# Optimization experiments

Hardware: AMD Instinct MI355X
Metric: run time of the kernel (lower is better)

Reference implementation:

```python
import jax, jax.numpy as jnp
import numpy as np

MAX_K_QK = 64
MAX_K_V = 64
MAX_K_KNOW = 128


def threshold_gate(scores, tau, max_k):
    # scores: [B,S,N], tau: [B,S,1]
    raw = scores - tau
    gate = jnp.where(raw > 0, raw, 1e-08 * jnp.exp(raw))
    exp_gate = jnp.exp(gate) - 1.0
    k = min(max_k, scores.shape[-1])
    topk_vals, _ = jax.lax.top_k(exp_gate, k)
    threshold = topk_vals[:, :, -1:]
    exp_gate = jnp.where(exp_gate >= threshold, exp_gate, 0.0)
    gate_sum = exp_gate.sum(axis=-1, keepdims=True) + 1e-08
    gate_strength = jnp.tanh(exp_gate.max(axis=-1, keepdims=True))
    return exp_gate / gate_sum * gate_strength


def setup_inputs() -> dict:
    key = jax.random.key(0)
    ks = jax.random.split(key, 8)
    B, S, D = 2, 2048, 1024
    N_QK, N_V, N_KNOW = 4096, 4096, 8192
    scale = 0.02  # keep scores in a sane range for exp()
    return {
        "x": jax.random.normal(ks[0], (B, S, D), jnp.float32),
        "qk_emb": jax.random.normal(ks[1], (N_QK, D), jnp.float32) * scale,
        "v_emb": jax.random.normal(ks[2], (N_V, D), jnp.float32) * scale,
        "know_emb": jax.random.normal(ks[3], (N_KNOW, D), jnp.float32) * scale,
        "w_attn": jax.random.normal(ks[4], (D, 3), jnp.float32) * scale,
        "b_attn": jnp.zeros((3,), jnp.float32),
        "w_know": jax.random.normal(ks[5], (D, 1), jnp.float32) * scale,
        "b_know": jnp.zeros((1,), jnp.float32),
    }


def reference(x, qk_emb, v_emb, know_emb, w_attn, b_attn, w_know, b_know):
    # deterministic=True -> router dropout is identity
    # attention gates
    scores_qk = jnp.einsum("bsd,nd->bsn", x, qk_emb)
    scores_v = jnp.einsum("bsd,nd->bsn", x, v_emb)
    tau_all = x @ w_attn + b_attn  # [B,S,3]
    g_Q = threshold_gate(scores_qk, tau_all[:, :, 0:1], MAX_K_QK)
    g_K = threshold_gate(scores_qk, tau_all[:, :, 1:2], MAX_K_QK)
    g_V = threshold_gate(scores_v, tau_all[:, :, 2:3], MAX_K_V)
    t_qk = 1.0 / qk_emb.shape[0]
    t_v = 1.0 / v_emb.shape[0]
    aux_attn = (
        ((g_Q.mean(axis=(0, 1)) - t_qk) ** 2).sum() * g_Q.shape[-1]
        + ((g_K.mean(axis=(0, 1)) - t_qk) ** 2).sum() * g_K.shape[-1]
        + ((g_V.mean(axis=(0, 1)) - t_v) ** 2).sum() * g_V.shape[-1]
    )
    # knowledge gates
    scores_know = jnp.einsum("bsd,nd->bsn", x, know_emb)
    tau_know = x @ w_know + b_know  # [B,S,1]
    g_know = threshold_gate(scores_know, tau_know, MAX_K_KNOW)
    t_know = 1.0 / know_emb.shape[0]
    aux_know = ((g_know.mean(axis=(0, 1)) - t_know) ** 2).sum() * g_know.shape[-1]
    return (g_Q, g_K, g_V, aux_attn, g_know, aux_know)
```

## Files before the change

kernel.cpp:

```cpp
#include <hip/hip_runtime.h>
#include <hip/hip_bf16.h>


#define M_ROWS 4096
#define DIM    1024
#define N_QK   4096
#define N_KNOW 8192

typedef unsigned short ushortT;
typedef __attribute__((ext_vector_type(8)))  short short8;
typedef __attribute__((ext_vector_type(16))) float f32x16;

__global__ __launch_bounds__(256) void tau_kernel(
    const float* __restrict__ x, const float* __restrict__ w_attn,
    const float* __restrict__ b_attn, const float* __restrict__ w_know,
    const float* __restrict__ b_know, float* __restrict__ tau4, int D)
{
    __shared__ float s_f[4][4];
    const int row = blockIdx.x;
    const int tid = threadIdx.x;
    const float* xr = x + (size_t)row * D;
    float p0 = 0.f, p1 = 0.f, p2 = 0.f, p3 = 0.f;
    for (int d = tid; d < D; d += 256) {
        float xv = xr[d];
        p0 += xv * w_attn[d * 3 + 0];
        p1 += xv * w_attn[d * 3 + 1];
        p2 += xv * w_attn[d * 3 + 2];
        p3 += xv * w_know[d];
    }
#pragma unroll
    for (int o = 32; o > 0; o >>= 1) {
        p0 += __shfl_down(p0, o, 64);
        p1 += __shfl_down(p1, o, 64);
        p2 += __shfl_down(p2, o, 64);
        p3 += __shfl_down(p3, o, 64);
    }
    const int lane = tid & 63, wv = tid >> 6;
    if (lane == 0) { s_f[wv][0] = p0; s_f[wv][1] = p1; s_f[wv][2] = p2; s_f[wv][3] = p3; }
    __syncthreads();
    if (tid < 4) {
        float v = s_f[0][tid] + s_f[1][tid] + s_f[2][tid] + s_f[3][tid];
        v += (tid < 3) ? b_attn[tid] : b_know[0];
        tau4[(size_t)row * 4 + tid] = v;
    }
}

__device__ __forceinline__ void split4(const float4 v, uint2& H, uint2& L) {
    float vv[4] = {v.x, v.y, v.z, v.w};
    unsigned h[4], l[4];
#pragma unroll
    for (int i = 0; i < 4; i++) {
        __hip_bfloat16 hb = __float2bfloat16(vv[i]);
        float r = vv[i] - __bfloat162float(hb);
        __hip_bfloat16 lb = __float2bfloat16(r);
        h[i] = *(ushortT*)&hb;
        l[i] = *(ushortT*)&lb;
    }
    H.x = h[0] | (h[1] << 16); H.y = h[2] | (h[3] << 16);
    L.x = l[0] | (l[1] << 16); L.y = l[2] | (l[3] << 16);
}

__global__ __launch_bounds__(256) void convertA(
    const float* __restrict__ src, ushortT* __restrict__ dst, int nElem4)
{
    int g = blockIdx.x * 256 + threadIdx.x;
    if (g >= nElem4) return;
    int row = g >> 8;
    int c4  = g & 255;
    int chunk = c4 >> 3, pos = c4 & 7;
    const float4 v = *(const float4*)(src + (size_t)row * DIM + c4 * 4);
    uint2 H, L;
    split4(v, H, L);
    ushortT* base = dst + (size_t)row * 2048 + chunk * 64;
    *(uint2*)(base + pos * 4)      = H;
    *(uint2*)(base + 32 + pos * 4) = L;
}

__global__ __launch_bounds__(512, 2) void gemm_fused4(
    const ushortT* __restrict__ Aext, const ushortT* __restrict__ Bext,
    float* __restrict__ gQ, float* __restrict__ gV, float* __restrict__ gKn,
    int nb0)
{
    extern __shared__ ushortT lds[];
#define ABUF(b) (lds + (b) * 32768)
#define BBUF(b) (lds + (b) * 32768 + 16384)
    const int tid = threadIdx.x;
    const int wave = tid >> 6, lane = tid & 63;
    const int l32 = lane & 31, h = lane >> 5;
    const int rx7 = l32 & 7;
    const int wm = (wave >> 2) * 128;
    const int wn = (wave & 3) * 64;
    const long long m0 = (long long)blockIdx.y * 256;
    const int nblk = nb0 + blockIdx.x;

    float* C; long long ldc; long long n0;
    if (nblk < 16)      { C = gQ;  ldc = N_QK;   n0 = (long long)nblk * 256; }
    else if (nblk < 32) { C = gV;  ldc = N_QK;   n0 = (long long)(nblk - 16) * 256; }
    else                { C = gKn; ldc = N_KNOW; n0 = (long long)(nblk - 32) * 256; }

    const ushortT* gAp[4]; const ushortT* gBp[4]; int lOff[4];
#pragma unroll
    for (int it = 0; it < 4; ++it) {
        int f = it * 512 + tid;
        int r = f >> 3, sp = f & 7;
        int sg = sp ^ (r & 7);
        gAp[it] = Aext + (m0 + r) * 2048 + sg * 8;
        gBp[it] = Bext + ((long long)blockIdx.x * 256 + r) * 2048 + sg * 8;
        lOff[it] = f * 8;
    }

    f32x16 acc[4][2] = {};

#define STAGE(buf, c) do {                                                         \
    _Pragma("unroll")                                                              \
    for (int it = 0; it < 4; ++it) {                                               \
        __builtin_amdgcn_global_load_lds(                                          \
            (const __attribute__((address_space(1))) unsigned*)(const void*)(gAp[it] + (c) * 64), \
            (__attribute__((address_space(3))) unsigned*)(void*)(ABUF(buf) + lOff[it]), 16, 0, 0); \
        __builtin_amdgcn_global_load_lds(                                          \
            (const __attribute__((address_space(1))) unsigned*)(const void*)(gBp[it] + (c) * 64), \
            (__attribute__((address_space(3))) unsigned*)(void*)(BBUF(buf) + lOff[it]), 16, 0, 0); \
    }                                                                              \
} while (0)

#define COMPUTE(buf) do {                                                          \
    _Pragma("unroll")                                                              \
    for (int kb = 0; kb < 2; ++kb) {                                               \
        const int so = ((kb * 2 + h) ^ rx7) * 16;                                  \
        short8 aH[4], aL[4], bH[2], bL[2];                                         \
        _Pragma("unroll")                                                          \
        for (int t = 0; t < 4; ++t) {                                              \
            const char* pa = (const char*)ABUF(buf) + (wm + t * 32 + l32) * 128;   \
            aH[t] = *(const short8*)(pa + so);                                     \
            aL[t] = *(const short8*)(pa + (so ^ 64));                              \
        }                                                                          \
        _Pragma("unroll")                                                          \
        for (int t = 0; t < 2; ++t) {                                              \
            const char* pb = (const char*)BBUF(buf) + (wn + t * 32 + l32) * 128;   \
            bH[t] = *(const short8*)(pb + so);                                     \
            bL[t] = *(const short8*)(pb + (so ^ 64));                              \
        }                                                                          \
        _Pragma("unroll")                                                          \
        for (int i = 0; i < 4; ++i)                                                \
            _Pragma("unroll")                                                      \
            for (int j = 0; j < 2; ++j) {                                          \
                acc[i][j] = __builtin_amdgcn_mfma_f32_32x32x16_bf16(aH[i], bH[j], acc[i][j], 0, 0, 0); \
                acc[i][j] = __builtin_amdgcn_mfma_f32_32x32x16_bf16(aH[i], bL[j], acc[i][j], 0, 0, 0); \
                acc[i][j] = __builtin_amdgcn_mfma_f32_32x32x16_bf16(aL[i], bH[j], acc[i][j], 0, 0, 0); \
                acc[i][j] = __builtin_amdgcn_mfma_f32_32x32x16_bf16(aL[i], bL[j], acc[i][j], 0, 0, 0); \
            }                                                                      \
    }                                                                              \
} while (0)

    STAGE(0, 0);
    STAGE(1, 1);

    for (int c = 0; c < 32; ++c) {
        if (c < 31) asm volatile("s_waitcnt vmcnt(8)" ::: "memory");
        else        asm volatile("s_waitcnt vmcnt(0)" ::: "memory");
        __builtin_amdgcn_s_barrier();
        __builtin_amdgcn_sched_barrier(0);
        COMPUTE(c & 1);
        __builtin_amdgcn_s_barrier();
        __builtin_amdgcn_sched_barrier(0);
        if (c + 2 < 32) STAGE(c & 1, c + 2);
    }
#undef STAGE
#undef COMPUTE
#undef ABUF
#undef BBUF

#pragma unroll
    for (int ti = 0; ti < 4; ++ti)
#pragma unroll
        for (int tj = 0; tj < 2; ++tj) {
            long long col = n0 + wn + tj * 32 + l32;
            long long rb  = m0 + wm + ti * 32 + 4 * h;
#pragma unroll
            for (int reg = 0; reg < 16; ++reg) {
                long long row = rb + (reg & 3) + 8 * (reg >> 2);
                C[row * ldc + col] = acc[ti][tj][reg];
            }
        }
}

__global__ __launch_bounds__(256) void gemm_fused2(
    const ushortT* __restrict__ Aext, const float* __restrict__ qk_emb,
    const float* __restrict__ v_emb, const float* __restrict__ know_emb,
    float* __restrict__ gQ, float* __restrict__ gV, float* __restrict__ gKn,
    long long rowOff)
{
    __shared__ ushortT AHL[128 * 64];
    __shared__ ushortT BHL[128 * 64];
    const int tid = threadIdx.x;
    const int wave = tid >> 6, lane = tid & 63;
    const int l32 = lane & 31, h = lane >> 5;
    const int rx7 = l32 & 7;
    const int wm = (wave >> 1) * 64, wn = (wave & 1) * 64;
    const long long m0 = (long long)blockIdx.y * 128;
    const int nblk = blockIdx.x;

    const float* Bsrc; float* C; long long ldc; long long n0;
    if (nblk < 32)      { Bsrc = qk_emb;   C = gQ;  ldc = N_QK;   n0 = (long long)nblk * 128; }
    else if (nblk < 64) { Bsrc = v_emb;    C = gV;  ldc = N_QK;   n0 = (long long)(nblk - 32) * 128; }
    else                { Bsrc = know_emb; C = gKn; ldc = N_KNOW; n0 = (long long)(nblk - 64) * 128; }

    const ushortT* gAp[4]; ushortT* lAp[4];
    const float*   gBp[4]; int offH[4], offL[4];
#pragma unroll
    for (int it = 0; it < 4; ++it) {
        int f = it * 256 + tid;
        int r = f >> 3, sp = f & 7;
        int sg = sp ^ (r & 7);
        gAp[it] = Aext + (m0 + r) * 2048 + sg * 8;
        lAp[it] = AHL + f * 8;
        int c4 = f & 7;
        int s = c4 >> 1, hf = c4 & 1;
        offH[it] = r * 128 + ((s ^ (r & 7)) * 16) + hf * 8;
        offL[it] = r * 128 + (((4 | s) ^ (r & 7)) * 16) + hf * 8;
        gBp[it] = Bsrc + (n0 + r) * DIM + c4 * 4;
    }
    const char* pA[2]; const char* pB[2];
#pragma unroll
    for (int t = 0; t < 2; ++t) {
        pA[t] = (const char*)AHL + (wm + t * 32 + l32) * 128;
        pB[t] = (const char*)BHL + (wn + t * 32 + l32) * 128;
    }

    f32x16 acc[2][2] = {};
    float4 bufB[4];
#pragma unroll
    for (int it = 0; it < 4; ++it) bufB[it] = *(const float4*)(gBp[it]);

    for (int c = 0; c < 32; ++c) {
#pragma unroll
        for (int it = 0; it < 4; ++it) {
            __builtin_amdgcn_global_load_lds(
                (const __attribute__((address_space(1))) unsigned*)(const void*)(gAp[it] + c * 64),
                (__attribute__((address_space(3))) unsigned*)(void*)lAp[it], 16, 0, 0);
            uint2 H, L;
            split4(bufB[it], H, L);
            *(uint2*)((char*)BHL + offH[it]) = H;
            *(uint2*)((char*)BHL + offL[it]) = L;
        }
        __syncthreads();
        if (c + 1 < 32) {
#pragma unroll
            for (int it = 0; it < 4; ++it)
                bufB[it] = *(const float4*)(gBp[it] + (c + 1) * 32);
        }
#pragma unroll
        for (int kb = 0; kb < 2; ++kb) {
            const int so = ((kb * 2 + h) ^ rx7) * 16;
            short8 aH[2], aL[2], bH[2], bL[2];
#pragma unroll
            for (int t = 0; t < 2; ++t) {
                aH[t] = *(const short8*)(pA[t] + so);
                aL[t] = *(const short8*)(pA[t] + (so ^ 64));
                bH[t] = *(const short8*)(pB[t] + so);
                bL[t] = *(const short8*)(pB[t] + (so ^ 64));
            }
#pragma unroll
            for (int i = 0; i < 2; ++i)
#pragma unroll
                for (int j = 0; j < 2; ++j) {
                    acc[i][j] = __builtin_amdgcn_mfma_f32_32x32x16_bf16(aH[i], bH[j], acc[i][j], 0, 0, 0);
                    acc[i][j] = __builtin_amdgcn_mfma_f32_32x32x16_bf16(aH[i], bL[j], acc[i][j], 0, 0, 0);
                    acc[i][j] = __builtin_amdgcn_mfma_f32_32x32x16_bf16(aL[i], bH[j], acc[i][j], 0, 0, 0);
                    acc[i][j] = __builtin_amdgcn_mfma_f32_32x32x16_bf16(aL[i], bL[j], acc[i][j], 0, 0, 0);
                }
        }
        __syncthreads();
    }
#pragma unroll
    for (int ti = 0; ti < 2; ++ti)
#pragma unroll
        for (int tj = 0; tj < 2; ++tj) {
            long long col = n0 + wn + tj * 32 + l32;
            long long rb  = rowOff + m0 + wm + ti * 32 + 4 * h;
#pragma unroll
            for (int reg = 0; reg < 16; ++reg) {
                long long row = rb + (reg & 3) + 8 * (reg >> 2);
                C[row * ldc + col] = acc[ti][tj][reg];
            }
        }
}

__device__ __forceinline__ unsigned floatToKey(float f) {
    unsigned b = __float_as_uint(f);
    return (b & 0x80000000u) ? ~b : (b | 0x80000000u);
}
__device__ __forceinline__ float keyToFloat(unsigned key) {
    unsigned b = (key & 0x80000000u) ? (key & 0x7FFFFFFFu) : ~key;
    return __uint_as_float(b);
}
__device__ __forceinline__ float egate(float raw) {
    float g = raw > 0.f ? raw : 1e-8f * __expf(raw);
    return expf(g) - 1.f;
}

template <int NV, bool VLOAD, bool VSTORE>
__device__ __forceinline__ void gate_body(
    const float* __restrict__ srow, float tA, float tB, bool hasB, int ksel,
    float* __restrict__ orowA, float* __restrict__ orowB,
    float* __restrict__ colA, float* __restrict__ colB,
    int* s_hist, unsigned* s_u, float* s_f)
{
    const int tid = threadIdx.x, lane = tid & 63, wv = tid >> 6;

    unsigned keys[NV * 4];
    unsigned kmax = 0u;
    float fs = 0.f, fq = 0.f;
#pragma unroll
    for (int i = 0; i < NV; i++) {
        float v0, v1, v2, v3;
        if (VLOAD) {
            float4 v = *(const float4*)(srow + (size_t)(i * 256 + tid) * 4);
            v0 = v.x; v1 = v.y; v2 = v.z; v3 = v.w;
        } else {
            v0 = srow[(i * 4 + 0) * 256 + tid];
            v1 = srow[(i * 4 + 1) * 256 + tid];
            v2 = srow[(i * 4 + 2) * 256 + tid];
            v3 = srow[(i * 4 + 3) * 256 + tid];
        }
        fs += v0 + v1 + v2 + v3;
        fq += v0 * v0 + v1 * v1 + v2 * v2 + v3 * v3;
        unsigned a = floatToKey(v0), b = floatToKey(v1);
        unsigned c = floatToKey(v2), d = floatToKey(v3);
        keys[i * 4 + 0] = a; keys[i * 4 + 1] = b;
        keys[i * 4 + 2] = c; keys[i * 4 + 3] = d;
        unsigned m1 = a > b ? a : b, m2 = c > d ? c : d;
        m1 = m1 > m2 ? m1 : m2;
        kmax = kmax > m1 ? kmax : m1;
    }
#pragma unroll
    for (int o = 32; o > 0; o >>= 1) {
        unsigned x = __shfl_down(kmax, o, 64);
        kmax = kmax > x ? kmax : x;
        fs += __shfl_down(fs, o, 64);
        fq += __shfl_down(fq, o, 64);
    }
    if (lane == 0) { s_u[wv] = kmax; s_f[wv] = fs; s_f[4 + wv] = fq; }
    __syncthreads();
    { unsigned a = s_u[0], b = s_u[1], c = s_u[2], d = s_u[3];
      unsigned m1 = a > b ? a : b, m2 = c > d ? c : d; kmax = m1 > m2 ? m1 : m2; }
    fs = s_f[0] + s_f[1] + s_f[2] + s_f[3];
    fq = s_f[4] + s_f[5] + s_f[6] + s_f[7];

    const float NT = (float)(NV * 4 * 256);
    const float mu = fs / NT;
    const float sd = sqrtf(fmaxf(fq / NT - mu * mu, 0.f));
    const unsigned pk = floatToKey(mu + 2.0f * sd);
    __syncthreads();

    int pc = 0;
#pragma unroll
    for (int i = 0; i < NV * 4; i++) pc += (keys[i] >= pk) ? 1 : 0;
#pragma unroll
    for (int o = 32; o > 0; o >>= 1) pc += __shfl_down(pc, o, 64);
    if (lane == 0) s_u[wv] = (unsigned)pc;
    __syncthreads();
    const int ptot = (int)(s_u[0] + s_u[1] + s_u[2] + s_u[3]);
    const unsigned filt = (ptot >= ksel) ? pk : 0u;

    unsigned prefix = 0u;
    int kk = ksel;
#pragma unroll
    for (int rnd = 0; rnd < 4; ++rnd) {
        const int sh = 24 - 8 * rnd;
        s_hist[tid] = 0;
        __syncthreads();
#pragma unroll
        for (int i = 0; i < NV * 4; i++) {
            unsigned key = keys[i];
            if (key >= filt && (((key ^ prefix) >> sh) >> 8) == 0u)
                atomicAdd(&s_hist[(key >> sh) & 255u], 1);
        }
        __syncthreads();
        if (tid < 64) {
            const int b3 = 255 - 4 * tid;
            const int h0 = s_hist[b3],     h1 = s_hist[b3 - 1];
            const int h2 = s_hist[b3 - 2], h3 = s_hist[b3 - 3];
            const int gsum = h0 + h1 + h2 + h3;
            int inc = gsum;
#pragma unroll
            for (int o = 1; o < 64; o <<= 1) {
                int v = __shfl_up(inc, o, 64);
                if (tid >= o) inc += v;
            }
            const int above = inc - gsum;
            const int c0 = above + h0, c1 = c0 + h1, c2 = c1 + h2, c3 = c2 + h3;
            if (kk > above && kk <= c3) {
                unsigned byt; int nk;
                if (kk <= c0)      { byt = (unsigned)b3;       nk = kk - above; }
                else if (kk <= c1) { byt = (unsigned)(b3 - 1); nk = kk - c0; }
                else if (kk <= c2) { byt = (unsigned)(b3 - 2); nk = kk - c1; }
                else               { byt = (unsigned)(b3 - 3); nk = kk - c2; }
                s_u[0] = byt; s_u[1] = (unsigned)nk;
            }
        }
        __syncthreads();
        prefix |= s_u[0] << sh;
        kk = (int)s_u[1];
    }
    const unsigned vk = prefix;

    float sA = 0.f, sB = 0.f;
#pragma unroll
    for (int i = 0; i < NV * 4; i++) {
        if (keys[i] >= vk) {
            float s = keyToFloat(keys[i]);
            sA += egate(s - tA);
            if (hasB) sB += egate(s - tB);
        }
    }
#pragma unroll
    for (int o = 32; o > 0; o >>= 1) {
        sA += __shfl_down(sA, o, 64);
        sB += __shfl_down(sB, o, 64);
    }
    if (lane == 0) { s_f[wv] = sA; s_f[4 + wv] = sB; }
    __syncthreads();
    sA = s_f[0] + s_f[1] + s_f[2] + s_f[3];
    sB = s_f[4] + s_f[5] + s_f[6] + s_f[7];

    const float smax = keyToFloat(kmax);
    const float scaleA = tanhf(egate(smax - tA)) / (sA + 1e-8f);
    const float scaleB = hasB ? tanhf(egate(smax - tB)) / (sB + 1e-8f) : 0.f;

#pragma unroll
    for (int i = 0; i < NV; i++) {
        float ga[4], gb[4];
        int eidx[4];
#pragma unroll
        for (int j = 0; j < 4; j++) {
            int ii = i * 4 + j;
            int idx = VLOAD ? (i * 1024 + tid * 4 + j) : (ii * 256 + tid);
            eidx[j] = idx;
            unsigned key = keys[ii];
            float vA = 0.f, vB = 0.f;
            if (key >= vk) {
                float s = keyToFloat(key);
                vA = egate(s - tA) * scaleA;
                atomicAdd(&colA[idx], vA);
                if (hasB) { vB = egate(s - tB) * scaleB; atomicAdd(&colB[idx], vB); }
            }
            ga[j] = vA; gb[j] = vB;
        }
        if (VSTORE) {
            *(float4*)(orowA + (size_t)eidx[0]) = make_float4(ga[0], ga[1], ga[2], ga[3]);
            if (hasB) *(float4*)(orowB + (size_t)eidx[0]) = make_float4(gb[0], gb[1], gb[2], gb[3]);
        } else {
#pragma unroll
            for (int j = 0; j < 4; j++) {
                orowA[eidx[j]] = ga[j];
                if (hasB) orowB[eidx[j]] = gb[j];
            }
        }
    }
}

__global__ __launch_bounds__(256) void gate_all(
    const float* __restrict__ tau4,
    float* __restrict__ gQ, float* __restrict__ gK,
    float* __restrict__ gV, float* __restrict__ gKn,
    float* __restrict__ colsums)
{
    __shared__ int s_hist[256];
    __shared__ unsigned s_u[4];
    __shared__ float s_f[8];
    const int bid = blockIdx.x;
    if (bid < 4096) {
        const int row = bid;
        const float t = tau4[(size_t)row * 4 + 3];
        gate_body<8, false, false>(
            gKn + (size_t)row * N_KNOW, t, 0.f, false, 128,
            gKn + (size_t)row * N_KNOW, nullptr,
            colsums + 3 * N_QK, nullptr, s_hist, s_u, s_f);
    } else if (bid < 8192) {
        const int row = bid - 4096;
        const float tA = tau4[(size_t)row * 4 + 0];
        const float tB = tau4[(size_t)row * 4 + 1];
        gate_body<4, true, true>(
            gQ + (size_t)row * N_QK, tA, tB, true, 64,
            gQ + (size_t)row * N_QK, gK + (size_t)row * N_QK,
            colsums, colsums + N_QK, s_hist, s_u, s_f);
    } else {
        const int row = bid - 8192;
        const float t = tau4[(size_t)row * 4 + 2];
        gate_body<4, true, true>(
            gV + (size_t)row * N_QK, t, 0.f, false, 64,
            gV + (size_t)row * N_QK, nullptr,
            colsums + 2 * N_QK, nullptr, s_hist, s_u, s_f);
    }
}

__global__ __launch_bounds__(256) void aux_kernel(
    const float* __restrict__ colsum,
    float* __restrict__ auxAttn, float* __restrict__ auxKnow)
{
    __shared__ float s_a[4];
    __shared__ float s_b[4];
    const int tid = threadIdx.x;
    const int lane = tid & 63, wv = tid >> 6;
    const float invM = 1.f / 4096.f;

    float sa = 0.f;
    const float tqk = 1.f / 4096.f;
    for (int i = tid; i < 3 * N_QK; i += 256) {
        float m = colsum[i] * invM - tqk;
        sa += m * m;
    }
    float sk = 0.f;
    const float tkn = 1.f / 8192.f;
    for (int i = tid; i < N_KNOW; i += 256) {
        float m = colsum[3 * N_QK + i] * invM - tkn;
        sk += m * m;
    }
#pragma unroll
    for (int o = 32; o > 0; o >>= 1) {
        sa += __shfl_down(sa, o, 64);
        sk += __shfl_down(sk, o, 64);
    }
    if (lane == 0) { s_a[wv] = sa; s_b[wv] = sk; }
    __syncthreads();
    if (tid == 0) {
        auxAttn[0] = (s_a[0] + s_a[1] + s_a[2] + s_a[3]) * 4096.f;
        auxKnow[0] = (s_b[0] + s_b[1] + s_b[2] + s_b[3]) * 8192.f;
    }
}

static void convert_b_range(const float* qk, const float* v, const float* kn,
                            ushortT* Bext, long long rowLo, long long rowHi,
                            hipStream_t stream)
{
    struct Seg { const float* p; long long lo, hi; };
    Seg seg[3] = { {qk, 0, 4096}, {v, 4096, 8192}, {kn, 8192, 16384} };
    for (int i = 0; i < 3; ++i) {
        long long lo = rowLo > seg[i].lo ? rowLo : seg[i].lo;
        long long hi = rowHi < seg[i].hi ? rowHi : seg[i].hi;
        if (lo < hi) {
            int nel4 = (int)((hi - lo) * 256);
            convertA<<<(nel4 + 255) / 256, 256, 0, stream>>>(
                seg[i].p + (size_t)(lo - seg[i].lo) * DIM,
                Bext + (size_t)(lo - rowLo) * 2048, nel4);
        }
    }
}

extern "C" void kernel_launch(void* const* d_in, const int* in_sizes, int n_in,
                              void* d_out, int out_size, void* d_ws, size_t ws_size,
                              hipStream_t stream)
{
    const float* x        = (const float*)d_in[0];
    const float* qk_emb   = (const float*)d_in[1];
    const float* v_emb    = (const float*)d_in[2];
    const float* know_emb = (const float*)d_in[3];
    const float* w_attn   = (const float*)d_in[4];
    const float* b_attn   = (const float*)d_in[5];
    const float* w_know   = (const float*)d_in[6];
    const float* b_know   = (const float*)d_in[7];
    float* out = (float*)d_out;

    const long long M = M_ROWS;

    float* gQ   = out;
    float* gK   = gQ + (size_t)M * N_QK;
    float* gV   = gK + (size_t)M * N_QK;
    float* auxA = gV + (size_t)M * N_QK;
    float* gKn  = auxA + 1;
    float* auxK = gKn + (size_t)M * N_KNOW;

    const long long nColsum = 3 * N_QK + N_KNOW;
    const long long tail_bytes = (M * 4 + nColsum) * 4;
    long long tailStart = ((long long)ws_size - tail_bytes) & ~255LL;
    float* tau4 = (float*)((char*)d_ws + tailStart);
    float* colsums = tau4 + (size_t)M * 4;

    const long long rowB = 4096;
    const long long aBytes = M * rowB;

    hipMemsetAsync(colsums, 0, nColsum * sizeof(float), stream);
    tau_kernel<<<(int)M, 256, 0, stream>>>(x, w_attn, b_attn, w_know, b_know, tau4, DIM);

    long long availB = tailStart - aBytes;
    long long nbc = availB > 0 ? availB / (256 * rowB) : 0;
    if (nbc > 64) nbc = 64;

    if (nbc >= 16) {
        ushortT* A_ext = (ushortT*)d_ws;
        ushortT* B_ext = (ushortT*)((char*)d_ws + aBytes);
        convertA<<<(int)(M * 256 / 256), 256, 0, stream>>>(x, A_ext, (int)(M * 256));
        for (long long nb0 = 0; nb0 < 64; nb0 += nbc) {
            long long nn = (64 - nb0 < nbc) ? (64 - nb0) : nbc;
            convert_b_range(qk_emb, v_emb, know_emb, B_ext,
                            nb0 * 256, (nb0 + nn) * 256, stream);
            gemm_fused4<<<dim3((unsigned)nn, 16), 512, 131072, stream>>>(
                A_ext, B_ext, gQ, gV, gKn, (int)nb0);
        }
    } else {
        long long ra = (tailStart / rowB / 128) * 128;
        if (ra > M) ra = M;
        if (ra < 128) ra = 128;
        ushortT* A_ext = (ushortT*)d_ws;
        for (long long a0 = 0; a0 < M; a0 += ra) {
            long long ac = (M - a0 < ra) ? (M - a0) : ra;
            int nel4 = (int)(ac * 256);
            convertA<<<(nel4 + 255) / 256, 256, 0, stream>>>(x + a0 * DIM, A_ext, nel4);
            gemm_fused2<<<dim3(128, (unsigned)(ac / 128)), 256, 0, stream>>>(
                A_ext, qk_emb, v_emb, know_emb, gQ, gV, gKn, a0);
        }
    }

    gate_all<<<12288, 256, 0, stream>>>(tau4, gQ, gK, gV, gKn, colsums);

    aux_kernel<<<1, 256, 0, stream>>>(colsums, auxA, auxK);
}
```

Before: 959.1 us.

## Split gate kernel into threshold search and wide apply pass; raise MFMA priority

```diff
diff --git a/kernel.cpp b/kernel.cpp
--- a/kernel.cpp
+++ b/kernel.cpp
@@ -140,6 +140,7 @@
             bH[t] = *(const short8*)(pb + so);                                     \
             bL[t] = *(const short8*)(pb + (so ^ 64));                              \
         }                                                                          \
+        __builtin_amdgcn_s_setprio(1);                                             \
         _Pragma("unroll")                                                          \
         for (int i = 0; i < 4; ++i)                                                \
             _Pragma("unroll")                                                      \
@@ -149,6 +150,7 @@
                 acc[i][j] = __builtin_amdgcn_mfma_f32_32x32x16_bf16(aL[i], bH[j], acc[i][j], 0, 0, 0); \
                 acc[i][j] = __builtin_amdgcn_mfma_f32_32x32x16_bf16(aL[i], bL[j], acc[i][j], 0, 0, 0); \
             }                                                                      \
+        __builtin_amdgcn_s_setprio(0);                                             \
     }                                                                              \
 } while (0)
 
@@ -299,11 +301,10 @@
     return expf(g) - 1.f;
 }
 
-template <int NV, bool VLOAD, bool VSTORE>
-__device__ __forceinline__ void gate_body(
+template <int NV, bool VLOAD>
+__device__ __forceinline__ void gate_search_body(
     const float* __restrict__ srow, float tA, float tB, bool hasB, int ksel,
-    float* __restrict__ orowA, float* __restrict__ orowB,
-    float* __restrict__ colA, float* __restrict__ colB,
+    float4* __restrict__ gparams, int prow,
     int* s_hist, unsigned* s_u, float* s_f)
 {
     const int tid = threadIdx.x, lane = tid & 63, wv = tid >> 6;
@@ -424,47 +425,18 @@
     sA = s_f[0] + s_f[1] + s_f[2] + s_f[3];
     sB = s_f[4] + s_f[5] + s_f[6] + s_f[7];
 
-    const float smax = keyToFloat(kmax);
-    const float scaleA = tanhf(egate(smax - tA)) / (sA + 1e-8f);
-    const float scaleB = hasB ? tanhf(egate(smax - tB)) / (sB + 1e-8f) : 0.f;
-
-#pragma unroll
-    for (int i = 0; i < NV; i++) {
-        float ga[4], gb[4];
-        int eidx[4];
-#pragma unroll
-        for (int j = 0; j < 4; j++) {
-            int ii = i * 4 + j;
-            int idx = VLOAD ? (i * 1024 + tid * 4 + j) : (ii * 256 + tid);
-            eidx[j] = idx;
-            unsigned key = keys[ii];
-            float vA = 0.f, vB = 0.f;
-            if (key >= vk) {
-                float s = keyToFloat(key);
-                vA = egate(s - tA) * scaleA;
-                atomicAdd(&colA[idx], vA);
-                if (hasB) { vB = egate(s - tB) * scaleB; atomicAdd(&colB[idx], vB); }
-            }
-            ga[j] = vA; gb[j] = vB;
-        }
-        if (VSTORE) {
-            *(float4*)(orowA + (size_t)eidx[0]) = make_float4(ga[0], ga[1], ga[2], ga[3]);
-            if (hasB) *(float4*)(orowB + (size_t)eidx[0]) = make_float4(gb[0], gb[1], gb[2], gb[3]);
-        } else {
-#pragma unroll
-            for (int j = 0; j < 4; j++) {
-                orowA[eidx[j]] = ga[j];
-                if (hasB) orowB[eidx[j]] = gb[j];
-            }
-        }
-    }
-}
-
-__global__ __launch_bounds__(256) void gate_all(
+    if (tid == 0) {
+        const float smax = keyToFloat(kmax);
+        const float scaleA = tanhf(egate(smax - tA)) / (sA + 1e-8f);
+        const float scaleB = hasB ? tanhf(egate(smax - tB)) / (sB + 1e-8f) : 0.f;
+        gparams[prow] = make_float4(__uint_as_float(vk), scaleA, scaleB, 0.f);
+    }
+}
+
+__global__ __launch_bounds__(256) void gate_search(
     const float* __restrict__ tau4,
-    float* __restrict__ gQ, float* __restrict__ gK,
-    float* __restrict__ gV, float* __restrict__ gKn,
-    float* __restrict__ colsums)
+    const float* __restrict__ gQ, const float* __restrict__ gV,
+    const float* __restrict__ gKn, float4* __restrict__ gparams)
 {
     __shared__ int s_hist[256];
     __shared__ unsigned s_u[4];
@@ -473,25 +445,101 @@
     if (bid < 4096) {
         const int row = bid;
         const float t = tau4[(size_t)row * 4 + 3];
-        gate_body<8, false, false>(
+        gate_search_body<8, false>(
             gKn + (size_t)row * N_KNOW, t, 0.f, false, 128,
-            gKn + (size_t)row * N_KNOW, nullptr,
-            colsums + 3 * N_QK, nullptr, s_hist, s_u, s_f);
+            gparams, row, s_hist, s_u, s_f);
     } else if (bid < 8192) {
         const int row = bid - 4096;
         const float tA = tau4[(size_t)row * 4 + 0];
         const float tB = tau4[(size_t)row * 4 + 1];
-        gate_body<4, true, true>(
+        gate_search_body<4, true>(
             gQ + (size_t)row * N_QK, tA, tB, true, 64,
-            gQ + (size_t)row * N_QK, gK + (size_t)row * N_QK,
-            colsums, colsums + N_QK, s_hist, s_u, s_f);
+            gparams, 4096 + row, s_hist, s_u, s_f);
     } else {
         const int row = bid - 8192;
         const float t = tau4[(size_t)row * 4 + 2];
-        gate_body<4, true, true>(
+        gate_search_body<4, true>(
             gV + (size_t)row * N_QK, t, 0.f, false, 64,
-            gV + (size_t)row * N_QK, nullptr,
-            colsums + 2 * N_QK, nullptr, s_hist, s_u, s_f);
+            gparams, 8192 + row, s_hist, s_u, s_f);
+    }
+}
+
+__global__ __launch_bounds__(256) void gate_apply(
+    const float4* __restrict__ gparams, const float* __restrict__ tau4,
+    float* __restrict__ gQ, float* __restrict__ gK,
+    float* __restrict__ gV, float* __restrict__ gKn,
+    float* __restrict__ colsums)
+{
+    const int b = blockIdx.x, tid = threadIdx.x;
+    if (b < 32768) {
+        const int row = b >> 3, sub = b & 7;
+        const float4 p = gparams[row];
+        const unsigned vk = __float_as_uint(p.x);
+        const float scale = p.y;
+        const float t = tau4[(size_t)row * 4 + 3];
+        float* base = gKn + (size_t)row * N_KNOW + sub * 1024;
+        float* cs = colsums + 3 * N_QK + sub * 1024;
+        const int i0 = tid * 4;
+#pragma unroll
+        for (int j = 0; j < 4; ++j) {
+            const int idx = i0 + j;
+            const float s = base[idx];
+            float vA = 0.f;
+            if (floatToKey(s) >= vk) {
+                vA = egate(s - t) * scale;
+                atomicAdd(&cs[idx], vA);
+            }
+            base[idx] = vA;
+        }
+    } else if (b < 49152) {
+        const int bb = b - 32768;
+        const int row = bb >> 2, sub = bb & 3;
+        const float4 p = gparams[4096 + row];
+        const unsigned vk = __float_as_uint(p.x);
+        const float scA = p.y, scB = p.z;
+        const float tA = tau4[(size_t)row * 4 + 0];
+        const float tB = tau4[(size_t)row * 4 + 1];
+        const int off = sub * 1024 + tid * 4;
+        float* qrow = gQ + (size_t)row * N_QK + off;
+        float* krow = gK + (size_t)row * N_QK + off;
+        const float4 v = *(const float4*)qrow;
+        float sv[4] = {v.x, v.y, v.z, v.w};
+        float a4[4], b4[4];
+#pragma unroll
+        for (int j = 0; j < 4; ++j) {
+            float vA = 0.f, vB = 0.f;
+            if (floatToKey(sv[j]) >= vk) {
+                vA = egate(sv[j] - tA) * scA;
+                vB = egate(sv[j] - tB) * scB;
+                atomicAdd(&colsums[off + j], vA);
+                atomicAdd(&colsums[N_QK + off + j], vB);
+            }
+            a4[j] = vA; b4[j] = vB;
+        }
+        *(float4*)qrow = make_float4(a4[0], a4[1], a4[2], a4[3]);
+        *(float4*)krow = make_float4(b4[0], b4[1], b4[2], b4[3]);
+    } else {
+        const int bb = b - 49152;
+        const int row = bb >> 2, sub = bb & 3;
+        const float4 p = gparams[8192 + row];
+        const unsigned vk = __float_as_uint(p.x);
+        const float scale = p.y;
+        const float t = tau4[(size_t)row * 4 + 2];
+        const int off = sub * 1024 + tid * 4;
+        float* vrow = gV + (size_t)row * N_QK + off;
+        const float4 v = *(const float4*)vrow;
+        float sv[4] = {v.x, v.y, v.z, v.w};
+        float a4[4];
+#pragma unroll
+        for (int j = 0; j < 4; ++j) {
+            float vA = 0.f;
+            if (floatToKey(sv[j]) >= vk) {
+                vA = egate(sv[j] - t) * scale;
+                atomicAdd(&colsums[2 * N_QK + off + j], vA);
+            }
+            a4[j] = vA;
+        }
+        *(float4*)vrow = make_float4(a4[0], a4[1], a4[2], a4[3]);
     }
 }
 
@@ -572,10 +620,12 @@
     float* auxK = gKn + (size_t)M * N_KNOW;
 
     const long long nColsum = 3 * N_QK + N_KNOW;
-    const long long tail_bytes = (M * 4 + nColsum) * 4;
+    const long long nParam4 = 12288;
+    const long long tail_bytes = (M * 4 + nColsum) * 4 + nParam4 * 16;
     long long tailStart = ((long long)ws_size - tail_bytes) & ~255LL;
     float* tau4 = (float*)((char*)d_ws + tailStart);
     float* colsums = tau4 + (size_t)M * 4;
+    float4* gparams = (float4*)(colsums + nColsum);
 
     const long long rowB = 4096;
     const long long aBytes = M * rowB;
@@ -612,7 +662,8 @@
         }
     }
 
-    gate_all<<<12288, 256, 0, stream>>>(tau4, gQ, gK, gV, gKn, colsums);
+    gate_search<<<12288, 256, 0, stream>>>(tau4, gQ, gV, gKn, gparams);
+    gate_apply<<<65536, 256, 0, stream>>>(gparams, tau4, gQ, gK, gV, gKn, colsums);
 
     aux_kernel<<<1, 256, 0, stream>>>(colsums, auxA, auxK);
 }
```

After: 1.041 ms. 1.09x slower.
